# Kernel optimization log

Measured on AMD Instinct MI355X. Metric: run time of the kernel, lower is better.

Reference implementation:

```python
import jax, jax.numpy as jnp
import numpy as np

D_MODEL = 1024
N_HEAD = 16
HEAD_DIM = D_MODEL // N_HEAD


def setup_inputs() -> dict:
    key = jax.random.key(0)
    ks = jax.random.split(key, 5)
    s_attn = 1.0 / np.sqrt(D_MODEL)
    s_proj = 1.0 / np.sqrt(D_MODEL)
    return {
        "x": jax.random.normal(ks[0], (4, 2048, D_MODEL), dtype=jnp.float32),
        "w_attn": jax.random.normal(ks[1], (D_MODEL, 3 * D_MODEL), dtype=jnp.float32) * s_attn,
        "b_attn": jax.random.normal(ks[2], (3 * D_MODEL,), dtype=jnp.float32) * 0.02,
        "w_proj": jax.random.normal(ks[3], (D_MODEL, D_MODEL), dtype=jnp.float32) * s_proj,
        "b_proj": jax.random.normal(ks[4], (D_MODEL,), dtype=jnp.float32) * 0.02,
    }


def reference(x, w_attn, b_attn, w_proj, b_proj):
    B, T, C = x.shape
    qkv = x @ w_attn + b_attn  # [B,T,3C]
    q, k, v = jnp.split(qkv, 3, axis=2)
    # [B,T,C] -> [B,H,T,Dh]
    def heads(t):
        return t.reshape(B, T, N_HEAD, HEAD_DIM).transpose(0, 2, 1, 3)
    q, k, v = heads(q), heads(k), heads(v)
    scale = 1.0 / np.sqrt(HEAD_DIM)
    att = jnp.einsum("bhqd,bhkd->bhqk", q, k) * scale
    att = jax.nn.softmax(att, axis=-1)  # NOTE: no causal mask in source
    y = jnp.einsum("bhqk,bhkd->bhqd", att, v)
    y = y.transpose(0, 2, 1, 3).reshape(B, T, C)
    return y @ w_proj + b_proj
```

## Files before the change

### kernel.cpp

```cpp
#include <hip/hip_runtime.h>
#include <hip/hip_bf16.h>
#include <cstdint>
#include <cstddef>

#define DI __device__ __forceinline__

typedef float f32x4 __attribute__((ext_vector_type(4)));
typedef short short8 __attribute__((ext_vector_type(8)));
typedef unsigned short us4 __attribute__((ext_vector_type(4)));
typedef unsigned int u32x2 __attribute__((ext_vector_type(2)));

constexpr int Bc = 4, Tc = 2048, Cc = 1024, Hc = 16, Dhc = 64;
constexpr int Mrows = Bc * Tc;
constexpr int N1 = 3 * Cc;
constexpr int K1 = Cc;

DI unsigned short f2bf(float f) {
  unsigned u = __builtin_bit_cast(unsigned, f);
  unsigned r = u + 0x7FFFu + ((u >> 16) & 1u);
  return (unsigned short)(r >> 16);
}
DI float bf2f(unsigned short h) {
  return __builtin_bit_cast(float, (unsigned)h << 16);
}
DI unsigned cvtpk(float a, float b) {
  unsigned r;
  asm("v_cvt_pk_bf16_f32 %0, %1, %2" : "=v"(r) : "v"(a), "v"(b));
  return r;
}

#define GLOAD16(gp, lp)                                                        \
  __builtin_amdgcn_global_load_lds(                                            \
      (const __attribute__((address_space(1))) void*)(gp),                     \
      (__attribute__((address_space(3))) void*)(lp), 16, 0, 0)

__global__ __launch_bounds__(256) void k_cast_x(const float* __restrict__ x,
                                                unsigned short* __restrict__ xb) {
  int i = (blockIdx.x * 256 + threadIdx.x) * 8;
  f32x4 a = *reinterpret_cast<const f32x4*>(x + i);
  f32x4 b = *reinterpret_cast<const f32x4*>(x + i + 4);
  us4 r0 = {f2bf(a[0]), f2bf(a[1]), f2bf(a[2]), f2bf(a[3])};
  us4 r1 = {f2bf(b[0]), f2bf(b[1]), f2bf(b[2]), f2bf(b[3])};
  *reinterpret_cast<us4*>(xb + i) = r0;
  *reinterpret_cast<us4*>(xb + i + 4) = r1;
}

__global__ __launch_bounds__(256) void k_transpose_bf(const float* __restrict__ w,
                                                      unsigned short* __restrict__ wT,
                                                      int Kd, int Nd) {
  __shared__ float t[64][65];
  int kb = blockIdx.y * 64, nb = blockIdx.x * 64;
  int c = threadIdx.x & 63, r4 = threadIdx.x >> 6;
#pragma unroll
  for (int it = 0; it < 16; ++it) {
    int r = it * 4 + r4;
    t[r][c] = w[(size_t)(kb + r) * Nd + nb + c];
  }
  __syncthreads();
#pragma unroll
  for (int it = 0; it < 16; ++it) {
    int r = it * 4 + r4;
    wT[(size_t)(nb + r) * Kd + kb + c] = f2bf(t[c][r]);
  }
}

__global__ __launch_bounds__(256) void k_transpose_split(const float* __restrict__ w,
                                                         unsigned short* __restrict__ whi,
                                                         unsigned short* __restrict__ wlo) {
  __shared__ float t[64][65];
  int kb = blockIdx.y * 64, nb = blockIdx.x * 64;
  int c = threadIdx.x & 63, r4 = threadIdx.x >> 6;
#pragma unroll
  for (int it = 0; it < 16; ++it) {
    int r = it * 4 + r4;
    t[r][c] = w[(size_t)(kb + r) * Cc + nb + c];
  }
  __syncthreads();
#pragma unroll
  for (int it = 0; it < 16; ++it) {
    int r = it * 4 + r4;
    float v = t[c][r];
    unsigned short hi = f2bf(v);
    float rem = v - bf2f(hi);
    size_t idx = (size_t)(nb + r) * Cc + kb + c;
    whi[idx] = hi;
    wlo[idx] = f2bf(rem);
  }
}

__global__ __launch_bounds__(256) void k_gemm_qkv(
    const unsigned short* __restrict__ xb, const unsigned short* __restrict__ waT,
    const float* __restrict__ bias, unsigned short* __restrict__ q,
    unsigned short* __restrict__ kkp, unsigned short* __restrict__ vT) {
  __shared__ unsigned short lA[128 * 64];
  __shared__ unsigned short lB[128 * 64];
  const int tid = threadIdx.x, lane = tid & 63, wid = tid >> 6;
  const int wr = wid >> 1, wc = wid & 1;
  const int l15 = lane & 15, l4 = lane >> 4;
  const int rowBase = blockIdx.y * 128;
  const int colBase = blockIdx.x * 128;

  f32x4 acc[4][4] = {};

  for (int kt = 0; kt < K1 / 64; ++kt) {
    __syncthreads();
#pragma unroll
    for (int ch = 0; ch < 4; ++ch) {
      int d = wid * 4096 + ch * 1024 + lane * 16;
      int r = d >> 7;
      int cbyte = (d & 127) ^ ((r & 7) << 4);
      const unsigned short* ga = xb + (size_t)(rowBase + r) * K1 + kt * 64 + (cbyte >> 1);
      GLOAD16(ga, (char*)lA + wid * 4096 + ch * 1024);
      const unsigned short* gb = waT + (size_t)(colBase + r) * K1 + kt * 64 + (cbyte >> 1);
      GLOAD16(gb, (char*)lB + wid * 4096 + ch * 1024);
    }
    __syncthreads();
#pragma unroll
    for (int ks = 0; ks < 2; ++ks) {
      short8 af[4], bfv[4];
#pragma unroll
      for (int mf = 0; mf < 4; ++mf) {
        int r = wr * 64 + mf * 16 + l15;
        af[mf] = *reinterpret_cast<const short8*>(
            (const char*)lA + r * 128 + ((ks * 64 + (l4 << 4)) ^ ((r & 7) << 4)));
      }
#pragma unroll
      for (int nf = 0; nf < 4; ++nf) {
        int r = wc * 64 + nf * 16 + l15;
        bfv[nf] = *reinterpret_cast<const short8*>(
            (const char*)lB + r * 128 + ((ks * 64 + (l4 << 4)) ^ ((r & 7) << 4)));
      }
#pragma unroll
      for (int mf = 0; mf < 4; ++mf)
#pragma unroll
        for (int nf = 0; nf < 4; ++nf)
          acc[mf][nf] = __builtin_amdgcn_mfma_f32_16x16x32_bf16(af[mf], bfv[nf],
                                                                acc[mf][nf], 0, 0, 0);
    }
  }
  const int sec = colBase >> 10;
#pragma unroll
  for (int nf = 0; nf < 4; ++nf) {
    int ccol = colBase + wc * 64 + nf * 16 + l15;
    float bv = bias[ccol];
    int cc = ccol & 1023;
    int h = cc >> 6, dd = cc & 63;
#pragma unroll
    for (int mf = 0; mf < 4; ++mf) {
      int r0 = rowBase + wr * 64 + mf * 16 + l4 * 4;
      f32x4 v = acc[mf][nf];
      if (sec == 2) {
        int b_ = r0 >> 11, t = r0 & 2047;
        int pair = b_ * 16 + h;
        us4 pk = {f2bf(v[0] + bv), f2bf(v[1] + bv), f2bf(v[2] + bv), f2bf(v[3] + bv)};
        *reinterpret_cast<us4*>(vT + ((size_t)pair * 64 + dd) * 2048 + t) = pk;
      } else {
        unsigned short* dst = (sec == 0) ? q : kkp;
#pragma unroll
        for (int j = 0; j < 4; ++j) {
          int r = r0 + j;
          int b_ = r >> 11, t = r & 2047;
          dst[((size_t)(b_ * 16 + h) * 2048 + t) * 64 + dd] = f2bf(v[j] + bv);
        }
      }
    }
  }
}

__global__ __launch_bounds__(256) void k_attn(
    const unsigned short* __restrict__ q, const unsigned short* __restrict__ kkp,
    const unsigned short* __restrict__ vT, unsigned short* __restrict__ yh,
    unsigned short* __restrict__ yl) {
  __shared__ unsigned short lK[64 * 64];
  __shared__ unsigned short lV[64 * 64];
  __shared__ unsigned short lP[4][32 * 64];
  const int tid = threadIdx.x, lane = tid & 63, wid = tid >> 6;
  const int l15 = lane & 15, l4 = lane >> 4;
  const int qb = blockIdx.x, pair = blockIdx.y;
  const size_t base = (size_t)pair * Tc * Dhc;
  const int swz = (l15 & 7) << 4;

  short8 qf[2][2];
#pragma unroll
  for (int qt = 0; qt < 2; ++qt) {
    int qrow = qb * 128 + wid * 32 + qt * 16 + l15;
#pragma unroll
    for (int ks = 0; ks < 2; ++ks)
      qf[qt][ks] = *reinterpret_cast<const short8*>(q + base + (size_t)qrow * 64 +
                                                    ks * 32 + l4 * 8);
  }

  f32x4 yac[2][4] = {};
  float lsum[2] = {0.f, 0.f};
  constexpr float C1 = 0.18033688011112042f;
  char* lPw = (char*)lP[wid];

  for (int kb = 0; kb < Tc / 64; ++kb) {
    __syncthreads();
#pragma unroll
    for (int ch = 0; ch < 2; ++ch) {
      int d = wid * 2048 + ch * 1024 + lane * 16;
      int r = d >> 7;
      int cbyte = (d & 127) ^ ((r & 7) << 4);
      const unsigned short* gk = kkp + base + (size_t)(kb * 64 + r) * 64 + (cbyte >> 1);
      GLOAD16(gk, (char*)lK + wid * 2048 + ch * 1024);
      const unsigned short* gv = vT + base + (size_t)r * 2048 + kb * 64 + (cbyte >> 1);
      GLOAD16(gv, (char*)lV + wid * 2048 + ch * 1024);
    }
    __syncthreads();

#pragma unroll
    for (int nf = 0; nf < 4; ++nf) {
      int r = nf * 16 + l15;
      f32x4 s0 = {0.f, 0.f, 0.f, 0.f}, s1 = {0.f, 0.f, 0.f, 0.f};
#pragma unroll
      for (int ks = 0; ks < 2; ++ks) {
        short8 kf = *reinterpret_cast<const short8*>(
            (const char*)lK + r * 128 + ((ks * 64 + (l4 << 4)) ^ swz));
        s0 = __builtin_amdgcn_mfma_f32_16x16x32_bf16(kf, qf[0][ks], s0, 0, 0, 0);
        s1 = __builtin_amdgcn_mfma_f32_16x16x32_bf16(kf, qf[1][ks], s1, 0, 0, 0);
      }
      float p0 = __builtin_amdgcn_exp2f(s0[0] * C1);
      float p1 = __builtin_amdgcn_exp2f(s0[1] * C1);
      float p2 = __builtin_amdgcn_exp2f(s0[2] * C1);
      float p3 = __builtin_amdgcn_exp2f(s0[3] * C1);
      lsum[0] += (p0 + p1) + (p2 + p3);
      u32x2 w0 = {cvtpk(p0, p1), cvtpk(p2, p3)};
      *reinterpret_cast<u32x2*>(lPw + l15 * 128 + ((nf * 32 + l4 * 8) ^ swz)) = w0;
      p0 = __builtin_amdgcn_exp2f(s1[0] * C1);
      p1 = __builtin_amdgcn_exp2f(s1[1] * C1);
      p2 = __builtin_amdgcn_exp2f(s1[2] * C1);
      p3 = __builtin_amdgcn_exp2f(s1[3] * C1);
      lsum[1] += (p0 + p1) + (p2 + p3);
      u32x2 w1 = {cvtpk(p0, p1), cvtpk(p2, p3)};
      *reinterpret_cast<u32x2*>(lPw + (16 + l15) * 128 + ((nf * 32 + l4 * 8) ^ swz)) = w1;
    }
#pragma unroll
    for (int ks = 0; ks < 2; ++ks) {
      short8 pf0 = *reinterpret_cast<const short8*>(
          lPw + l15 * 128 + ((ks * 64 + (l4 << 4)) ^ swz));
      short8 pf1 = *reinterpret_cast<const short8*>(
          lPw + (16 + l15) * 128 + ((ks * 64 + (l4 << 4)) ^ swz));
#pragma unroll
      for (int mf = 0; mf < 4; ++mf) {
        int r = mf * 16 + l15;
        short8 vf = *reinterpret_cast<const short8*>(
            (const char*)lV + r * 128 + ((ks * 64 + (l4 << 4)) ^ swz));
        yac[0][mf] = __builtin_amdgcn_mfma_f32_16x16x32_bf16(vf, pf0, yac[0][mf], 0, 0, 0);
        yac[1][mf] = __builtin_amdgcn_mfma_f32_16x16x32_bf16(vf, pf1, yac[1][mf], 0, 0, 0);
      }
    }
  }
  const int b_ = pair >> 4, h = pair & 15;
#pragma unroll
  for (int qt = 0; qt < 2; ++qt) {
    float l = lsum[qt];
    l += __shfl_xor(l, 16);
    l += __shfl_xor(l, 32);
    float invl = 1.0f / l;
    size_t rowg = (size_t)(b_ * 2048 + qb * 128 + wid * 32 + qt * 16 + l15);
#pragma unroll
    for (int mf = 0; mf < 4; ++mf) {
      f32x4 v = yac[qt][mf];
      us4 hi, lo;
#pragma unroll
      for (int j = 0; j < 4; ++j) {
        float f = v[j] * invl;
        unsigned short h1 = f2bf(f);
        hi[j] = h1;
        lo[j] = f2bf(f - bf2f(h1));
      }
      size_t off = rowg * 1024 + h * 64 + mf * 16 + l4 * 4;
      *reinterpret_cast<us4*>(yh + off) = hi;
      *reinterpret_cast<us4*>(yl + off) = lo;
    }
  }
}

__global__ __launch_bounds__(256) void k_gemm_proj(
    const unsigned short* __restrict__ yh, const unsigned short* __restrict__ yl,
    const unsigned short* __restrict__ wph, const unsigned short* __restrict__ wpl,
    const float* __restrict__ bias, float* __restrict__ out) {
  __shared__ unsigned short lAh[64 * 64], lAl[64 * 64];
  __shared__ unsigned short lBh[128 * 64], lBl[128 * 64];
  const int tid = threadIdx.x, lane = tid & 63, wid = tid >> 6;
  const int wr = wid >> 1, wc = wid & 1;
  const int l15 = lane & 15, l4 = lane >> 4;
  const int rowBase = blockIdx.y * 64;
  const int colBase = blockIdx.x * 128;

  f32x4 acc[2][4] = {};

  for (int kt = 0; kt < 16; ++kt) {
    __syncthreads();
#pragma unroll
    for (int ch = 0; ch < 2; ++ch) {
      int d = wid * 2048 + ch * 1024 + lane * 16;
      int r = d >> 7;
      int cbyte = (d & 127) ^ ((r & 7) << 4);
      const unsigned short* gah = yh + (size_t)(rowBase + r) * Cc + kt * 64 + (cbyte >> 1);
      GLOAD16(gah, (char*)lAh + wid * 2048 + ch * 1024);
      const unsigned short* gal = yl + (size_t)(rowBase + r) * Cc + kt * 64 + (cbyte >> 1);
      GLOAD16(gal, (char*)lAl + wid * 2048 + ch * 1024);
    }
#pragma unroll
    for (int ch = 0; ch < 4; ++ch) {
      int d = wid * 4096 + ch * 1024 + lane * 16;
      int r = d >> 7;
      int cbyte = (d & 127) ^ ((r & 7) << 4);
      const unsigned short* gbh = wph + (size_t)(colBase + r) * Cc + kt * 64 + (cbyte >> 1);
      GLOAD16(gbh, (char*)lBh + wid * 4096 + ch * 1024);
      const unsigned short* gbl = wpl + (size_t)(colBase + r) * Cc + kt * 64 + (cbyte >> 1);
      GLOAD16(gbl, (char*)lBl + wid * 4096 + ch * 1024);
    }
    __syncthreads();
#pragma unroll
    for (int ks = 0; ks < 2; ++ks) {
      short8 ah[2], al_[2], bh[4], bl[4];
#pragma unroll
      for (int mf = 0; mf < 2; ++mf) {
        int r = wr * 32 + mf * 16 + l15;
        int off = r * 128 + ((ks * 64 + (l4 << 4)) ^ ((r & 7) << 4));
        ah[mf] = *reinterpret_cast<const short8*>((const char*)lAh + off);
        al_[mf] = *reinterpret_cast<const short8*>((const char*)lAl + off);
      }
#pragma unroll
      for (int nf = 0; nf < 4; ++nf) {
        int r = wc * 64 + nf * 16 + l15;
        int off = r * 128 + ((ks * 64 + (l4 << 4)) ^ ((r & 7) << 4));
        bh[nf] = *reinterpret_cast<const short8*>((const char*)lBh + off);
        bl[nf] = *reinterpret_cast<const short8*>((const char*)lBl + off);
      }
#pragma unroll
      for (int mf = 0; mf < 2; ++mf)
#pragma unroll
        for (int nf = 0; nf < 4; ++nf) {
          acc[mf][nf] = __builtin_amdgcn_mfma_f32_16x16x32_bf16(ah[mf], bh[nf],
                                                                acc[mf][nf], 0, 0, 0);
          acc[mf][nf] = __builtin_amdgcn_mfma_f32_16x16x32_bf16(ah[mf], bl[nf],
                                                                acc[mf][nf], 0, 0, 0);
          acc[mf][nf] = __builtin_amdgcn_mfma_f32_16x16x32_bf16(al_[mf], bh[nf],
                                                                acc[mf][nf], 0, 0, 0);
        }
    }
  }
#pragma unroll
  for (int nf = 0; nf < 4; ++nf) {
    int c = colBase + wc * 64 + nf * 16 + l15;
    float bv = bias[c];
#pragma unroll
    for (int mf = 0; mf < 2; ++mf) {
      int r0 = rowBase + wr * 32 + mf * 16 + l4 * 4;
      f32x4 v = acc[mf][nf];
#pragma unroll
      for (int j = 0; j < 4; ++j) out[(size_t)(r0 + j) * Cc + c] = v[j] + bv;
    }
  }
}

extern "C" void kernel_launch(void* const* d_in, const int* in_sizes, int n_in,
                              void* d_out, int out_size, void* d_ws, size_t ws_size,
                              hipStream_t stream) {
  const float* x = (const float*)d_in[0];
  const float* w_attn = (const float*)d_in[1];
  const float* b_attn = (const float*)d_in[2];
  const float* w_proj = (const float*)d_in[3];
  const float* b_proj = (const float*)d_in[4];
  float* out = (float*)d_out;
  char* ws = (char*)d_ws;
  const size_t MiB = 1u << 20;
  unsigned short* xb = (unsigned short*)(ws + 0 * MiB);
  unsigned short* waT = (unsigned short*)(ws + 16 * MiB);
  unsigned short* q = (unsigned short*)(ws + 22 * MiB);
  unsigned short* kk = (unsigned short*)(ws + 38 * MiB);
  unsigned short* vT = (unsigned short*)(ws + 54 * MiB);
  unsigned short* yh = (unsigned short*)(ws + 70 * MiB);
  unsigned short* yl = (unsigned short*)(ws + 86 * MiB);
  unsigned short* wph = (unsigned short*)(ws + 102 * MiB);
  unsigned short* wpl = (unsigned short*)(ws + 104 * MiB);

  k_cast_x<<<dim3(4096), dim3(256), 0, stream>>>(x, xb);
  k_transpose_bf<<<dim3(48, 16), dim3(256), 0, stream>>>(w_attn, waT, K1, N1);
  k_transpose_split<<<dim3(16, 16), dim3(256), 0, stream>>>(w_proj, wph, wpl);
  k_gemm_qkv<<<dim3(24, 64), dim3(256), 0, stream>>>(xb, waT, b_attn, q, kk, vT);
  k_attn<<<dim3(16, 64), dim3(256), 0, stream>>>(q, kk, vT, yh, yl);
  k_gemm_proj<<<dim3(8, 128), dim3(256), 0, stream>>>(yh, yl, wph, wpl, b_proj, out);
}
```

Measured before the change: 321.2 us.

## Double-buffer K/V tiles in attention with 512-thread blocks and MFMA priority

The attention kernel now runs 8 waves of 512 threads per block, each covering 256 query rows, so every staged K/V tile is shared by twice as many waves. K and V tiles are double-buffered in LDS: the next tile's global load is issued right after a single barrier, so it overlaps the current tile's compute instead of sitting between two barriers. s_setprio is raised around the MFMA sections to favour matrix issue. The trade-offs are more LDS per block, which may lower occupancy, and only half as many blocks in the grid.

```diff
diff --git a/kernel.cpp b/kernel.cpp
--- a/kernel.cpp
+++ b/kernel.cpp
@@ -167,23 +167,29 @@
   }
 }
 
-__global__ __launch_bounds__(256) void k_attn(
+__global__ __launch_bounds__(512) void k_attn(
     const unsigned short* __restrict__ q, const unsigned short* __restrict__ kkp,
     const unsigned short* __restrict__ vT, unsigned short* __restrict__ yh,
     unsigned short* __restrict__ yl) {
-  __shared__ unsigned short lK[64 * 64];
-  __shared__ unsigned short lV[64 * 64];
-  __shared__ unsigned short lP[4][32 * 64];
+  __shared__ unsigned short lK[2][64 * 64];
+  __shared__ unsigned short lV[2][64 * 64];
+  __shared__ unsigned short lP[8][32 * 64];
   const int tid = threadIdx.x, lane = tid & 63, wid = tid >> 6;
   const int l15 = lane & 15, l4 = lane >> 4;
   const int qb = blockIdx.x, pair = blockIdx.y;
   const size_t base = (size_t)pair * Tc * Dhc;
   const int swz = (l15 & 7) << 4;
 
+  const int sd = wid * 1024 + lane * 16;
+  const int sr = sd >> 7;
+  const int scb = (sd & 127) ^ ((sr & 7) << 4);
+  const unsigned short* gkbase = kkp + base + (size_t)sr * 64 + (scb >> 1);
+  const unsigned short* gvbase = vT + base + (size_t)sr * 2048 + (scb >> 1);
+
   short8 qf[2][2];
 #pragma unroll
   for (int qt = 0; qt < 2; ++qt) {
-    int qrow = qb * 128 + wid * 32 + qt * 16 + l15;
+    int qrow = qb * 256 + wid * 32 + qt * 16 + l15;
 #pragma unroll
     for (int ks = 0; ks < 2; ++ks)
       qf[qt][ks] = *reinterpret_cast<const short8*>(q + base + (size_t)qrow * 64 +
@@ -195,31 +201,32 @@
   constexpr float C1 = 0.18033688011112042f;
   char* lPw = (char*)lP[wid];
 
+  GLOAD16(gkbase, (char*)lK[0] + wid * 1024);
+  GLOAD16(gvbase, (char*)lV[0] + wid * 1024);
+
   for (int kb = 0; kb < Tc / 64; ++kb) {
-    __syncthreads();
-#pragma unroll
-    for (int ch = 0; ch < 2; ++ch) {
-      int d = wid * 2048 + ch * 1024 + lane * 16;
-      int r = d >> 7;
-      int cbyte = (d & 127) ^ ((r & 7) << 4);
-      const unsigned short* gk = kkp + base + (size_t)(kb * 64 + r) * 64 + (cbyte >> 1);
-      GLOAD16(gk, (char*)lK + wid * 2048 + ch * 1024);
-      const unsigned short* gv = vT + base + (size_t)r * 2048 + kb * 64 + (cbyte >> 1);
-      GLOAD16(gv, (char*)lV + wid * 2048 + ch * 1024);
-    }
-    __syncthreads();
-
+    const int b = kb & 1;
+    asm volatile("s_waitcnt vmcnt(0)" ::: "memory");
+    __builtin_amdgcn_s_barrier();
+    if (kb < Tc / 64 - 1) {
+      GLOAD16(gkbase + (size_t)(kb + 1) * 4096, (char*)lK[b ^ 1] + wid * 1024);
+      GLOAD16(gvbase + (kb + 1) * 64, (char*)lV[b ^ 1] + wid * 1024);
+    }
+
+    const char* lKb = (const char*)lK[b];
 #pragma unroll
     for (int nf = 0; nf < 4; ++nf) {
       int r = nf * 16 + l15;
       f32x4 s0 = {0.f, 0.f, 0.f, 0.f}, s1 = {0.f, 0.f, 0.f, 0.f};
+      __builtin_amdgcn_s_setprio(1);
 #pragma unroll
       for (int ks = 0; ks < 2; ++ks) {
         short8 kf = *reinterpret_cast<const short8*>(
-            (const char*)lK + r * 128 + ((ks * 64 + (l4 << 4)) ^ swz));
+            lKb + r * 128 + ((ks * 64 + (l4 << 4)) ^ swz));
         s0 = __builtin_amdgcn_mfma_f32_16x16x32_bf16(kf, qf[0][ks], s0, 0, 0, 0);
         s1 = __builtin_amdgcn_mfma_f32_16x16x32_bf16(kf, qf[1][ks], s1, 0, 0, 0);
       }
+      __builtin_amdgcn_s_setprio(0);
       float p0 = __builtin_amdgcn_exp2f(s0[0] * C1);
       float p1 = __builtin_amdgcn_exp2f(s0[1] * C1);
       float p2 = __builtin_amdgcn_exp2f(s0[2] * C1);
@@ -235,6 +242,8 @@
       u32x2 w1 = {cvtpk(p0, p1), cvtpk(p2, p3)};
       *reinterpret_cast<u32x2*>(lPw + (16 + l15) * 128 + ((nf * 32 + l4 * 8) ^ swz)) = w1;
     }
+    const char* lVb = (const char*)lV[b];
+    __builtin_amdgcn_s_setprio(1);
 #pragma unroll
     for (int ks = 0; ks < 2; ++ks) {
       short8 pf0 = *reinterpret_cast<const short8*>(
@@ -245,11 +254,12 @@
       for (int mf = 0; mf < 4; ++mf) {
         int r = mf * 16 + l15;
         short8 vf = *reinterpret_cast<const short8*>(
-            (const char*)lV + r * 128 + ((ks * 64 + (l4 << 4)) ^ swz));
+            lVb + r * 128 + ((ks * 64 + (l4 << 4)) ^ swz));
         yac[0][mf] = __builtin_amdgcn_mfma_f32_16x16x32_bf16(vf, pf0, yac[0][mf], 0, 0, 0);
         yac[1][mf] = __builtin_amdgcn_mfma_f32_16x16x32_bf16(vf, pf1, yac[1][mf], 0, 0, 0);
       }
     }
+    __builtin_amdgcn_s_setprio(0);
   }
   const int b_ = pair >> 4, h = pair & 15;
 #pragma unroll
@@ -258,7 +268,7 @@
     l += __shfl_xor(l, 16);
     l += __shfl_xor(l, 32);
     float invl = 1.0f / l;
-    size_t rowg = (size_t)(b_ * 2048 + qb * 128 + wid * 32 + qt * 16 + l15);
+    size_t rowg = (size_t)(b_ * 2048 + qb * 256 + wid * 32 + qt * 16 + l15);
 #pragma unroll
     for (int mf = 0; mf < 4; ++mf) {
       f32x4 v = yac[qt][mf];
@@ -383,6 +393,6 @@
   k_transpose_bf<<<dim3(48, 16), dim3(256), 0, stream>>>(w_attn, waT, K1, N1);
   k_transpose_split<<<dim3(16, 16), dim3(256), 0, stream>>>(w_proj, wph, wpl);
   k_gemm_qkv<<<dim3(24, 64), dim3(256), 0, stream>>>(xb, waT, b_attn, q, kk, vT);
-  k_attn<<<dim3(16, 64), dim3(256), 0, stream>>>(q, kk, vT, yh, yl);
+  k_attn<<<dim3(8, 64), dim3(512), 0, stream>>>(q, kk, vT, yh, yl);
   k_gemm_proj<<<dim3(8, 128), dim3(256), 0, stream>>>(yh, yl, wph, wpl, b_proj, out);
 }
```

New measurement: 310.2 us. -3.4%, faster.
